# Optimization experiments

Measured on AMD Instinct MI355X. Metric: run time of the kernel, lower is better.

The kernel has to match this reference:

```python
import jax, jax.numpy as jnp
import numpy as np
import math

DIM = 256; SEQ = 2048; BSZ = 32; NI = 128; NS = 4; ITERS = 3

def _ln(x, g, b):
    m = x.mean(-1, keepdims=True)
    v = ((x - m) ** 2).mean(-1, keepdims=True)
    return (x - m) / jnp.sqrt(v + 1e-5) * g + b

def _norm(x):
    # torch F.normalize: x / ||x||.clamp_min(1e-12)
    return x / jnp.clip(jnp.linalg.norm(x, axis=-1, keepdims=True), 1e-12, None)

def setup_inputs() -> dict:
    key = jax.random.key(0)
    ks = jax.random.split(key, 16)
    def w(k, shape, s=0.02):
        return jax.random.normal(k, shape, jnp.float32) * s
    return {
        'tokens': jax.random.normal(ks[0], (BSZ, SEQ, DIM), jnp.float32),
        'cls_embed': jax.random.normal(ks[1], (BSZ, DIM), jnp.float32),
        'intent_queries': jax.random.normal(ks[2], (NI, DIM), jnp.float32),
        'noise': jax.random.normal(ks[3], (NI, BSZ, NS, DIM), jnp.float32),
        'Wk': w(ks[4], (DIM, DIM)), 'bk': jnp.zeros(DIM, jnp.float32),
        'Wv': w(ks[5], (DIM, DIM)), 'bv': jnp.zeros(DIM, jnp.float32),
        'Wqs': w(ks[6], (DIM, DIM)), 'bqs': jnp.zeros(DIM, jnp.float32),
        'Wqi': w(ks[7], (DIM, DIM)), 'bqi': jnp.zeros(DIM, jnp.float32),
        'ln1_g': jnp.ones(DIM, jnp.float32), 'ln1_b': jnp.zeros(DIM, jnp.float32),
        'ln2_g': jnp.ones(DIM, jnp.float32), 'ln2_b': jnp.zeros(DIM, jnp.float32),
        'Wf1': w(ks[8], (DIM, 2 * DIM)), 'bf1': jnp.zeros(2 * DIM, jnp.float32),
        'Wf2': w(ks[9], (2 * DIM, DIM)), 'bf2': jnp.zeros(DIM, jnp.float32),
        'slot_mu': w(ks[10], (1, NS, DIM)),  # randn*0.02
        'slot_sigma': jnp.ones((1, NS, DIM), jnp.float32) * 0.1,
        'alpha': jnp.float32(1.0),
        'temperature': jnp.float32(1.0),
    }

def reference(tokens, cls_embed, intent_queries, noise, Wk, bk, Wv, bv,
              Wqs, bqs, Wqi, bqi, ln1_g, ln1_b, ln2_g, ln2_b,
              Wf1, bf1, Wf2, bf2, slot_mu, slot_sigma, alpha, temperature):
    scale = 1.0 / math.sqrt(DIM)
    # k/v are identical across the per-intent loop in the original -> compute once
    k = tokens @ Wk + bk  # [B,S,D]
    v = tokens @ Wv + bv  # [B,S,D]
    cls_n = _norm(cls_embed)  # [B,D]

    def per_intent(q, eps):  # q: [D], eps: [B,NS,D]
        qn = _norm(q)
        q_intent = (q @ Wqi + bqi)[None, None, :]  # broadcast over [B,NS,:]
        slots = slot_mu[0] + eps * slot_sigma[0]   # [B,NS,D]
        for _ in range(ITERS):
            q_slot = slots @ Wqs + bqs + q_intent
            logit = jnp.einsum('bnd,bsd->bns', q_slot, k) * scale
            attn = jax.nn.softmax(logit, axis=-1)
            upd = jnp.einsum('bns,bsd->bnd', attn, v)
            slots = _ln(slots + upd, ln1_g, ln1_b)
            h = _ln(slots, ln2_g, ln2_b)
            slots = slots + jax.nn.gelu(h @ Wf1 + bf1, approximate=False) @ Wf2 + bf2
        sn = _norm(slots)                               # [B,NS,D]
        a = jax.nn.softmax(jnp.einsum('bnd,d->bn', sn, qn), axis=-1)
        summ = jnp.einsum('bn,bnd->bd', a, slots)       # slot_summary
        fused = cls_n + alpha * _norm(summ)
        return fused @ qn                               # [B]

    scores = jax.vmap(per_intent)(intent_queries, noise)  # [NI,B]
    logits = scores.T / jnp.maximum(temperature, 1e-4)    # [B,NI]
    return logits
```

## Files before the change

### kernel.cpp

```cpp
#include <hip/hip_runtime.h>
#include <math.h>

#define BSZ 32
#define NI  128

typedef __attribute__((ext_vector_type(8))) _Float16 f16x8;
typedef __attribute__((ext_vector_type(4))) _Float16 f16x4;
typedef __attribute__((ext_vector_type(4))) float    f32x4;

#define MFMA16(a, b, c) __builtin_amdgcn_mfma_f32_16x16x32_f16((a), (b), (c), 0, 0, 0)

#define GLL(g, l) __builtin_amdgcn_global_load_lds(                          \
    (const __attribute__((address_space(1))) void*)(g),                      \
    (__attribute__((address_space(3))) void*)(l), 16, 0, 0)

#define LGKM_BAR() do {                                                      \
    asm volatile("s_waitcnt lgkmcnt(0)" ::: "memory");                       \
    __builtin_amdgcn_sched_barrier(0);                                       \
    __builtin_amdgcn_s_barrier();                                            \
    __builtin_amdgcn_sched_barrier(0); } while (0)

__device__ inline float dot4f(float4 a, float4 b) {
    return a.x * b.x + a.y * b.y + a.z * b.z + a.w * b.w;
}

__device__ inline float4* slp(float* base, int r, int c) {
    return (float4*)(base + r * 256 + ((((c) >> 2) ^ (r & 7)) << 2));
}

__device__ inline void tpose64(const float* __restrict__ src, int Csrc,
                               _Float16* __restrict__ dstT, int KT,
                               int r0, int c0, _Float16 (*tbuf)[72], int tid)
{
#pragma unroll
    for (int it = 0; it < 4; it++) {
        int idx = tid + it * 256;
        int rr = idx >> 4, c4 = idx & 15;
        float4 w = *(const float4*)(src + (size_t)(r0 + rr) * Csrc + c0 + c4 * 4);
        tbuf[c4 * 4 + 0][rr] = (_Float16)w.x;
        tbuf[c4 * 4 + 1][rr] = (_Float16)w.y;
        tbuf[c4 * 4 + 2][rr] = (_Float16)w.z;
        tbuf[c4 * 4 + 3][rr] = (_Float16)w.w;
    }
    __syncthreads();
#pragma unroll
    for (int it = 0; it < 2; it++) {
        int idx = tid + it * 256;
        int orr = idx >> 3, oc8 = idx & 7;
        int n = c0 + orr;
        size_t tile = (size_t)(n >> 4) * KT + (r0 >> 5) + (oc8 >> 2);
        *(f16x8*)(dstT + tile * 512 + (n & 15) * 32 + (oc8 & 3) * 8) = *(const f16x8*)&tbuf[orr][oc8 * 8];
    }
}

__global__ __launch_bounds__(256) void prep(
    const float* __restrict__ Wk, const float* __restrict__ Wv,
    const float* __restrict__ Wqs, const float* __restrict__ Wf1,
    const float* __restrict__ Wf2,
    const float* __restrict__ intent_q, const float* __restrict__ Wqi,
    const float* __restrict__ bqi, const float* __restrict__ bqs,
    const float* __restrict__ cls_embed,
    _Float16* __restrict__ wkT, _Float16* __restrict__ wvT,
    _Float16* __restrict__ wqsT, _Float16* __restrict__ wf1T,
    _Float16* __restrict__ wf2T,
    float* __restrict__ qint2, float* __restrict__ qn, float* __restrict__ clsn)
{
    __shared__ _Float16 tbuf[64][72];
    __shared__ float buf[256];
    __shared__ float red[4];
    const int t = threadIdx.x, blk = blockIdx.x;
    const int lane = t & 63, w = t >> 6;

    if (blk < 112) {
        if (blk < 16)       tpose64(Wk, 256, wkT, 8, (blk >> 2) * 64, (blk & 3) * 64, tbuf, t);
        else if (blk < 32)  { int tt = blk - 16; tpose64(Wv, 256, wvT, 8, (tt >> 2) * 64, (tt & 3) * 64, tbuf, t); }
        else if (blk < 48)  { int tt = blk - 32; tpose64(Wqs, 256, wqsT, 8, (tt >> 2) * 64, (tt & 3) * 64, tbuf, t); }
        else if (blk < 80)  { int tt = blk - 48; tpose64(Wf1, 512, wf1T, 8, (tt & 3) * 64, (tt >> 2) * 64, tbuf, t); }
        else                { int tt = blk - 80; tpose64(Wf2, 256, wf2T, 16, (tt >> 2) * 64, (tt & 3) * 64, tbuf, t); }
    } else if (blk < 240) {
        int i = blk - 112;
        float x = intent_q[(size_t)i * 256 + t];
        buf[t] = x;
        float ss = x * x;
#pragma unroll
        for (int m = 1; m < 64; m <<= 1) ss += __shfl_xor(ss, m, 64);
        if (lane == 0) red[w] = ss;
        __syncthreads();
        float tot = red[0] + red[1] + red[2] + red[3];
        qn[(size_t)i * 256 + t] = x / fmaxf(sqrtf(tot), 1e-12f);
        float acc = bqi[t] + bqs[t];
        for (int e = 0; e < 256; e += 4) {
            const float4 q4 = *(const float4*)&buf[e];
            acc += q4.x * Wqi[(size_t)(e + 0) * 256 + t];
            acc += q4.y * Wqi[(size_t)(e + 1) * 256 + t];
            acc += q4.z * Wqi[(size_t)(e + 2) * 256 + t];
            acc += q4.w * Wqi[(size_t)(e + 3) * 256 + t];
        }
        qint2[(size_t)i * 256 + t] = acc;
    } else {
        int b = blk - 240;
        float x = cls_embed[(size_t)b * 256 + t];
        float ss = x * x;
#pragma unroll
        for (int m = 1; m < 64; m <<= 1) ss += __shfl_xor(ss, m, 64);
        if (lane == 0) red[w] = ss;
        __syncthreads();
        float tot = red[0] + red[1] + red[2] + red[3];
        clsn[(size_t)b * 256 + t] = x / fmaxf(sqrtf(tot), 1e-12f);
    }
}

__global__ __launch_bounds__(512, 2) void kvf_k(
    const float* __restrict__ tokens,
    const _Float16* __restrict__ wkT, const _Float16* __restrict__ wvT,
    const float* __restrict__ bk, const float* __restrict__ bv,
    _Float16* __restrict__ kT, _Float16* __restrict__ vT)
{
    __shared__ __align__(16) _Float16 Sb[2][8192];

    const int t = threadIdx.x, lane = t & 63, w = t >> 6;
    const int l15 = lane & 15, quad = lane >> 4;
    const int lofs = l15 * 32 + quad * 8;
    const int lofsA = ((l15 * 4 + quad) ^ ((l15 >> 1) & 7)) * 8;
    const int bx = blockIdx.x;
    const int b = bx & 31, chunk = bx >> 5;

    f16x8 wk[2][8], wv[2][8];
#pragma unroll
    for (int j = 0; j < 2; j++)
#pragma unroll
        for (int ks = 0; ks < 8; ks++) {
            wk[j][ks] = *(const f16x8*)(wkT + ((size_t)(2 * w + j) * 8 + ks) * 512 + lofs);
            wv[j][ks] = *(const f16x8*)(wvT + ((size_t)(2 * w + j) * 8 + ks) * 512 + lofs);
        }
    f32x4 bi0 = *(const f32x4*)(bk + w * 32 + quad * 4);
    f32x4 bi1 = *(const f32x4*)(bk + w * 32 + 16 + quad * 4);
    const float bv0 = bv[(2 * w) * 16 + l15];
    const float bv1 = bv[(2 * w + 1) * 16 + l15];

    const int rr = t >> 5, d8 = t & 31;
    const float* tbase = tokens + ((size_t)b * 2048 + chunk * 256) * 256 + rr * 256 + d8 * 8;
    const int mskW = ((rr >> 1) & 7) ^ (((d8 >> 2) & 3) << 1);
    const int wofs0 = (d8 >> 2) * 512 + (((rr * 4 + (d8 & 3)) ^ mskW) * 8);
    const int wofs1 = wofs0 + 8 * 512;

    float4 pa0, pa1, pb0, pb1;

#define KVF_LOADS(P) do {                                                    \
        const float* sp_ = tbase + (size_t)(P) * 8192;                       \
        pa0 = *(const float4*)(sp_);                                         \
        pa1 = *(const float4*)(sp_ + 4);                                     \
        pb0 = *(const float4*)(sp_ + 4096);                                  \
        pb1 = *(const float4*)(sp_ + 4100);                                  \
    } while (0)

#define KVF_STAGE(BUF) do {                                                  \
        f16x8 h0, h1;                                                        \
        h0[0] = (_Float16)pa0.x; h0[1] = (_Float16)pa0.y;                    \
        h0[2] = (_Float16)pa0.z; h0[3] = (_Float16)pa0.w;                    \
        h0[4] = (_Float16)pa1.x; h0[5] = (_Float16)pa1.y;                    \
        h0[6] = (_Float16)pa1.z; h0[7] = (_Float16)pa1.w;                    \
        h1[0] = (_Float16)pb0.x; h1[1] = (_Float16)pb0.y;                    \
        h1[2] = (_Float16)pb0.z; h1[3] = (_Float16)pb0.w;                    \
        h1[4] = (_Float16)pb1.x; h1[5] = (_Float16)pb1.y;                    \
        h1[6] = (_Float16)pb1.z; h1[7] = (_Float16)pb1.w;                    \
        *(f16x8*)((BUF) + wofs0) = h0;                                       \
        *(f16x8*)((BUF) + wofs1) = h1;                                       \
    } while (0)

    KVF_LOADS(0);
    KVF_STAGE(&Sb[0][0]);
    LGKM_BAR();

    for (int p = 0; p < 8; p++) {
        if (p < 7) KVF_LOADS(p + 1);
        __builtin_amdgcn_sched_barrier(0);

        const _Float16* lb = &Sb[p & 1][0];
        const int stg0 = chunk * 16 + p * 2;
        const int sp = chunk * 8 + p;

        f16x8 a[2][8];
#pragma unroll
        for (int st = 0; st < 2; st++)
#pragma unroll
            for (int ks = 0; ks < 8; ks++)
                a[st][ks] = *(const f16x8*)(lb + (st * 8 + ks) * 512 + (lofsA ^ ((ks & 3) * 16)));

#pragma unroll
        for (int st = 0; st < 2; st++) {
            f32x4 c0 = {0.f, 0.f, 0.f, 0.f}, c1 = {0.f, 0.f, 0.f, 0.f};
#pragma unroll
            for (int ks = 0; ks < 8; ks++) {
                c0 = MFMA16(wk[0][ks], a[st][ks], c0);
                c1 = MFMA16(wk[1][ks], a[st][ks], c1);
            }
            f16x4 p0, p1;
#pragma unroll
            for (int reg = 0; reg < 4; reg++) {
                p0[reg] = (_Float16)(c0[reg] + bi0[reg]);
                p1[reg] = (_Float16)(c1[reg] + bi1[reg]);
            }
            _Float16* tp = kT + ((size_t)(b * 128 + stg0 + st) * 8 + w) * 512 + l15 * 32;
            *(f16x4*)(tp + (quad >> 1) * 8 + (quad & 1) * 4) = p0;
            *(f16x4*)(tp + (2 + (quad >> 1)) * 8 + (quad & 1) * 4) = p1;
        }

#pragma unroll
        for (int j = 0; j < 2; j++) {
            f32x4 c0 = {0.f, 0.f, 0.f, 0.f}, c1 = {0.f, 0.f, 0.f, 0.f};
#pragma unroll
            for (int ks = 0; ks < 8; ks++) {
                c0 = MFMA16(a[0][ks], wv[j][ks], c0);
                c1 = MFMA16(a[1][ks], wv[j][ks], c1);
            }
            const float bb = j ? bv1 : bv0;
            f16x4 p0, p1;
#pragma unroll
            for (int reg = 0; reg < 4; reg++) {
                p0[reg] = (_Float16)(c0[reg] + bb);
                p1[reg] = (_Float16)(c1[reg] + bb);
            }
            _Float16* tp = vT + ((size_t)(b * 16 + 2 * w + j) * 64 + sp) * 512 + l15 * 32;
            *(f16x4*)(tp + (quad >> 1) * 8 + (quad & 1) * 4) = p0;
            *(f16x4*)(tp + (2 + (quad >> 1)) * 8 + (quad & 1) * 4) = p1;
        }

        if (p < 7) {
            KVF_STAGE(&Sb[(p + 1) & 1][0]);
            LGKM_BAR();
        }
    }
#undef KVF_LOADS
#undef KVF_STAGE
}

__global__ __launch_bounds__(256, 4) void slotq_k(
    const float* __restrict__ noise, const float* __restrict__ slot_mu,
    const float* __restrict__ slot_sigma,
    const _Float16* __restrict__ wqsT, const float* __restrict__ qint2,
    float* __restrict__ slots, _Float16* __restrict__ qsT)
{
    __shared__ float sb[16 * 256];
    const int tid = threadIdx.x, lane = tid & 63, w4 = tid >> 6;
    const int l15 = lane & 15, quad = lane >> 4;
    const int lofs = l15 * 32 + quad * 8;
    const int rt = blockIdx.x;
    const int gr0 = rt * 16;

    {
        const int lr = w4 * 4 + quad;
        const int gr = gr0 + lr;
        const int b = gr >> 9, i = (gr >> 2) & 127, n = gr & 3;
        const float* np = noise + (((size_t)i * BSZ + b) * 4 + n) * 256;
#pragma unroll
        for (int k = 0; k < 4; k++) {
            const int c = k * 64 + l15 * 4;
            float4 mu = *(const float4*)(slot_mu + n * 256 + c);
            float4 sg = *(const float4*)(slot_sigma + n * 256 + c);
            float4 ns = *(const float4*)(np + c);
            float4 o;
            o.x = mu.x + ns.x * sg.x; o.y = mu.y + ns.y * sg.y;
            o.z = mu.z + ns.z * sg.z; o.w = mu.w + ns.w * sg.w;
            *slp(sb, lr, c) = o;
            *(float4*)(slots + (size_t)gr * 256 + c) = o;
        }
    }
    __syncthreads();

    f16x8 bs[8];
#pragma unroll
    for (int ks = 0; ks < 8; ks++) {
        const int c0 = ks * 32 + quad * 8;
        float4 xa = *slp(sb, l15, c0);
        float4 xb = *slp(sb, l15, c0 + 4);
        bs[ks][0] = (_Float16)xa.x; bs[ks][1] = (_Float16)xa.y;
        bs[ks][2] = (_Float16)xa.z; bs[ks][3] = (_Float16)xa.w;
        bs[ks][4] = (_Float16)xb.x; bs[ks][5] = (_Float16)xb.y;
        bs[ks][6] = (_Float16)xb.z; bs[ks][7] = (_Float16)xb.w;
    }
    const int iq = ((gr0 + l15) & 511) >> 2;
#pragma unroll
    for (int d = 0; d < 4; d++) {
        const int dti = w4 * 4 + d;
        f32x4 c = {0.f, 0.f, 0.f, 0.f};
#pragma unroll
        for (int ks = 0; ks < 8; ks++)
            c = MFMA16(*(const f16x8*)(wqsT + ((size_t)dti * 8 + ks) * 512 + lofs), bs[ks], c);
        float4 qi = *(const float4*)(qint2 + (size_t)iq * 256 + dti * 16 + quad * 4);
        f16x4 o;
#pragma unroll
        for (int reg = 0; reg < 4; reg++) o[reg] = (_Float16)((c[reg] + qi[reg]) * 0.0625f);
        *(f16x4*)(qsT + ((size_t)rt * 8 + (dti >> 1)) * 512 + l15 * 32
                  + ((dti & 1) * 2 + (quad >> 1)) * 8 + (quad & 1) * 4) = o;
    }
}

__global__ __launch_bounds__(256, 2) void attn_k(
    const _Float16* __restrict__ qsT, const _Float16* __restrict__ kT,
    const _Float16* __restrict__ vT,
    _Float16* __restrict__ Opart, float* __restrict__ psum4)
{
    __shared__ __align__(16) _Float16 arena[24576];
    __shared__ __align__(16) _Float16 pb[4][1280];

    _Float16* KbA = arena;
    _Float16* VbA = arena + 16384;

    const int tid = threadIdx.x, lane = tid & 63, wv = tid >> 6;
    const int l15 = lane & 15, quad = lane >> 4;
    const int lofs = l15 * 32 + quad * 8;
    const int lofsA = ((l15 * 4 + quad) ^ ((l15 >> 1) & 7)) * 8;
    const int lnsw = (lane ^ ((lane >> 3) & 7)) * 8;
    const int bx = blockIdx.x;
    const int b = bx & 31, rb = (bx >> 5) & 3, sk = bx >> 7;
    const int gr0 = b * 512 + rb * 128 + wv * 32;
    const int rt_q = gr0 >> 4;

    _Float16* pw = pb[wv];

    const _Float16* kSrc = kT + ((size_t)(b * 128 + sk * 32) * 8) * 512;
    const _Float16* vSrc = vT + ((size_t)(b * 16) * 64 + sk * 16) * 512;

#pragma unroll
    for (int j = 0; j < 4; j++) {
        const int ee = wv * 4 + j;
        GLL(kSrc + (size_t)((ee >> 3) * 8 + (ee & 7)) * 512 + lnsw,
            KbA + ee * 512 + lane * 8);
    }

    f16x8 q[2][8];
#pragma unroll
    for (int m = 0; m < 2; m++)
#pragma unroll
        for (int ks = 0; ks < 8; ks++)
            q[m][ks] = *(const f16x8*)(qsT + ((size_t)(rt_q + m) * 8 + ks) * 512 + lofs);

    f32x4 O[2][16];
#pragma unroll
    for (int m = 0; m < 2; m++)
#pragma unroll
        for (int dt = 0; dt < 16; dt++) O[m][dt] = (f32x4){0.f, 0.f, 0.f, 0.f};
    float ps[2][4] = {{0.f, 0.f, 0.f, 0.f}, {0.f, 0.f, 0.f, 0.f}};

    asm volatile("s_waitcnt vmcnt(0)" ::: "memory");
    __builtin_amdgcn_s_barrier();
    __builtin_amdgcn_sched_barrier(0);

    for (int ss = 0; ss < 16; ss++) {
        const int cur = ss & 1;

#pragma unroll
        for (int j = 0; j < 4; j++) {
            const int ee = wv * 4 + j;
            GLL(vSrc + (size_t)(ee * 64 + ss) * 512 + lnsw, VbA + ee * 512 + lane * 8);
        }
        if (ss < 15) {
#pragma unroll
            for (int j = 0; j < 4; j++) {
                const int ee = wv * 4 + j;
                GLL(kSrc + (size_t)((2 * (ss + 1) + (ee >> 3)) * 8 + (ee & 7)) * 512 + lnsw,
                    KbA + (cur ^ 1) * 8192 + ee * 512 + lane * 8);
            }
            asm volatile("s_waitcnt vmcnt(8)" ::: "memory");
        } else {
            asm volatile("s_waitcnt vmcnt(4)" ::: "memory");
        }
        __builtin_amdgcn_s_barrier();
        __builtin_amdgcn_sched_barrier(0);

#pragma unroll
        for (int kt = 0; kt < 2; kt++) {
            const _Float16* kp = KbA + cur * 8192 + (kt * 8) * 512;
            f32x4 c0 = {0.f, 0.f, 0.f, 0.f}, c1 = {0.f, 0.f, 0.f, 0.f};
#pragma unroll
            for (int ks = 0; ks < 8; ks++) {
                f16x8 kf = *(const f16x8*)(kp + ks * 512 + lofsA);
                c0 = MFMA16(q[0][ks], kf, c0);
                c1 = MFMA16(q[1][ks], kf, c1);
            }
            const int col = kt * 16 + l15;
#pragma unroll
            for (int reg = 0; reg < 4; reg++) {
                float p0 = __expf(fminf(c0[reg], 10.5f));
                float p1 = __expf(fminf(c1[reg], 10.5f));
                ps[0][reg] += p0;
                ps[1][reg] += p1;
                pw[(quad * 4 + reg) * 40 + col] = (_Float16)p0;
                pw[(16 + quad * 4 + reg) * 40 + col] = (_Float16)p1;
            }
        }

        __builtin_amdgcn_sched_barrier(0);
        asm volatile("s_waitcnt lgkmcnt(0)" ::: "memory");
        if (ss < 15) {
            asm volatile("s_waitcnt vmcnt(4)" ::: "memory");
        } else {
            asm volatile("s_waitcnt vmcnt(0)" ::: "memory");
        }
        __builtin_amdgcn_s_barrier();
        __builtin_amdgcn_sched_barrier(0);

        {
            f16x8 pa0 = *(const f16x8*)(pw + l15 * 40 + quad * 8);
            f16x8 pa1 = *(const f16x8*)(pw + (16 + l15) * 40 + quad * 8);
#pragma unroll
            for (int dt = 0; dt < 16; dt++) {
                f16x8 vf = *(const f16x8*)(VbA + dt * 512 + lofsA);
                O[0][dt] = MFMA16(pa0, vf, O[0][dt]);
                O[1][dt] = MFMA16(pa1, vf, O[1][dt]);
            }
        }
        __builtin_amdgcn_sched_barrier(0);
        __builtin_amdgcn_s_barrier();
        __builtin_amdgcn_sched_barrier(0);
    }

#pragma unroll
    for (int m = 0; m < 2; m++) {
#pragma unroll
        for (int msk = 1; msk <= 8; msk <<= 1)
#pragma unroll
            for (int reg = 0; reg < 4; reg++) ps[m][reg] += __shfl_xor(ps[m][reg], msk, 64);
        if (l15 == 0) {
#pragma unroll
            for (int reg = 0; reg < 4; reg++)
                psum4[(size_t)sk * 16384 + gr0 + m * 16 + quad * 4 + reg] = ps[m][reg];
        }
    }

    _Float16* ow = arena + wv * 2176;
#pragma unroll
    for (int m = 0; m < 2; m++) {
#pragma unroll
        for (int hd = 0; hd < 2; hd++) {
#pragma unroll
            for (int dt = 0; dt < 8; dt++) {
                const int dti = hd * 8 + dt;
#pragma unroll
                for (int reg = 0; reg < 4; reg++)
                    ow[(quad * 4 + reg) * 136 + dt * 16 + l15] = (_Float16)O[m][dti][reg];
            }
#pragma unroll
            for (int p2 = 0; p2 < 4; p2++) {
                const int u = lane + p2 * 64;
                const int row = u >> 4, col8 = u & 15;
                *(f16x8*)(Opart + ((size_t)sk * 16384 + gr0 + m * 16 + row) * 256 + hd * 128 + col8 * 8) =
                    *(const f16x8*)(ow + row * 136 + col8 * 8);
            }
        }
    }
}

__global__ __launch_bounds__(256, 2) void mlp_k(
    const _Float16* __restrict__ Opart, const float* __restrict__ psum4,
    float* __restrict__ slots,
    const float* __restrict__ ln1_g, const float* __restrict__ ln1_b,
    const float* __restrict__ ln2_g, const float* __restrict__ ln2_b,
    const _Float16* __restrict__ wf1T, const float* __restrict__ bf1,
    const _Float16* __restrict__ wf2T, const float* __restrict__ bf2,
    const _Float16* __restrict__ wqsT, const float* __restrict__ qint2,
    _Float16* __restrict__ qsT,
    const float* __restrict__ qn, const float* __restrict__ clsn,
    const float* __restrict__ alphap, const float* __restrict__ tempp,
    float* __restrict__ out, int it)
{
    __shared__ float sl[32 * 256];
    __shared__ float2 st2[32];
    __shared__ __align__(16) _Float16 actL[16384];

    const int tid = threadIdx.x, lane = tid & 63, w4 = tid >> 6;
    const int l15 = lane & 15, quad = lane >> 4;
    const int lofs = l15 * 32 + quad * 8;
    const int lofsA = ((l15 * 4 + quad) ^ ((l15 >> 1) & 7)) * 8;
    const int bx = blockIdx.x;
    const int b = bx & 31, rg = bx >> 5;
    const int R0 = b * 512 + rg * 32;

#pragma unroll
    for (int r2 = 0; r2 < 2; r2++) {
        const int lr = w4 * 8 + r2 * 4 + quad;
        const int gr = R0 + lr;
        float l = 0.f;
#pragma unroll
        for (int j = 0; j < 4; j++) l += psum4[(size_t)j * 16384 + gr];
        const float invl = 1.f / l;
        float4 y[4];
        float sm = 0.f, sq = 0.f;
#pragma unroll
        for (int k = 0; k < 4; k++) {
            const int c = k * 64 + l15 * 4;
            float4 o4 = {0.f, 0.f, 0.f, 0.f};
#pragma unroll
            for (int j = 0; j < 4; j++) {
                f16x4 p = *(const f16x4*)(Opart + ((size_t)j * 16384 + gr) * 256 + c);
                o4.x += (float)p[0]; o4.y += (float)p[1];
                o4.z += (float)p[2]; o4.w += (float)p[3];
            }
            float4 s4 = *(const float4*)(slots + (size_t)gr * 256 + c);
            y[k].x = s4.x + o4.x * invl; y[k].y = s4.y + o4.y * invl;
            y[k].z = s4.z + o4.z * invl; y[k].w = s4.w + o4.w * invl;
            sm += y[k].x + y[k].y + y[k].z + y[k].w;
            sq += dot4f(y[k], y[k]);
        }
#pragma unroll
        for (int m = 1; m <= 8; m <<= 1) { sm += __shfl_xor(sm, m, 64); sq += __shfl_xor(sq, m, 64); }
        const float mean = sm * (1.f / 256.f);
        const float rstd = rsqrtf(sq * (1.f / 256.f) - mean * mean + 1e-5f);
        float sm2 = 0.f, sq2 = 0.f;
#pragma unroll
        for (int k = 0; k < 4; k++) {
            const int c = k * 64 + l15 * 4;
            float4 g1 = *(const float4*)(ln1_g + c);
            float4 b1 = *(const float4*)(ln1_b + c);
            float4 x1;
            x1.x = (y[k].x - mean) * rstd * g1.x + b1.x;
            x1.y = (y[k].y - mean) * rstd * g1.y + b1.y;
            x1.z = (y[k].z - mean) * rstd * g1.z + b1.z;
            x1.w = (y[k].w - mean) * rstd * g1.w + b1.w;
            *slp(sl, lr, c) = x1;
            sm2 += x1.x + x1.y + x1.z + x1.w;
            sq2 += dot4f(x1, x1);
        }
#pragma unroll
        for (int m = 1; m <= 8; m <<= 1) { sm2 += __shfl_xor(sm2, m, 64); sq2 += __shfl_xor(sq2, m, 64); }
        const float mean2 = sm2 * (1.f / 256.f);
        const float rstd2 = rsqrtf(sq2 * (1.f / 256.f) - mean2 * mean2 + 1e-5f);
        if (l15 == 0) st2[lr] = make_float2(mean2, rstd2);
    }
    __syncthreads();

    {
        f16x8 bh[2][8];
#pragma unroll
        for (int tt = 0; tt < 2; tt++) {
            const float2 s2 = st2[tt * 16 + l15];
#pragma unroll
            for (int ks = 0; ks < 8; ks++) {
                const int c0 = ks * 32 + quad * 8;
                float4 xa = *slp(sl, tt * 16 + l15, c0);
                float4 xb = *slp(sl, tt * 16 + l15, c0 + 4);
                float4 ga = *(const float4*)(ln2_g + c0);
                float4 gb = *(const float4*)(ln2_g + c0 + 4);
                float4 ba = *(const float4*)(ln2_b + c0);
                float4 bb2 = *(const float4*)(ln2_b + c0 + 4);
                bh[tt][ks][0] = (_Float16)((xa.x - s2.x) * s2.y * ga.x + ba.x);
                bh[tt][ks][1] = (_Float16)((xa.y - s2.x) * s2.y * ga.y + ba.y);
                bh[tt][ks][2] = (_Float16)((xa.z - s2.x) * s2.y * ga.z + ba.z);
                bh[tt][ks][3] = (_Float16)((xa.w - s2.x) * s2.y * ga.w + ba.w);
                bh[tt][ks][4] = (_Float16)((xb.x - s2.x) * s2.y * gb.x + bb2.x);
                bh[tt][ks][5] = (_Float16)((xb.y - s2.x) * s2.y * gb.y + bb2.y);
                bh[tt][ks][6] = (_Float16)((xb.z - s2.x) * s2.y * gb.z + bb2.z);
                bh[tt][ks][7] = (_Float16)((xb.w - s2.x) * s2.y * gb.w + bb2.w);
            }
        }
#pragma unroll 2
        for (int t8 = 0; t8 < 8; t8++) {
            const int hti = w4 * 8 + t8;
            f32x4 c0 = {0.f, 0.f, 0.f, 0.f}, c1 = {0.f, 0.f, 0.f, 0.f};
#pragma unroll
            for (int ks = 0; ks < 8; ks++) {
                f16x8 wfrag = *(const f16x8*)(wf1T + ((size_t)hti * 8 + ks) * 512 + lofs);
                c0 = MFMA16(wfrag, bh[0][ks], c0);
                c1 = MFMA16(wfrag, bh[1][ks], c1);
            }
            float4 bb = *(const float4*)(bf1 + hti * 16 + quad * 4);
            f16x4 o0, o1;
#pragma unroll
            for (int reg = 0; reg < 4; reg++) {
                float xg0 = c0[reg] + bb[reg];
                float xg1 = c1[reg] + bb[reg];
                o0[reg] = (_Float16)(0.5f * xg0 * (1.f + erff(xg0 * 0.70710678118654752f)));
                o1[reg] = (_Float16)(0.5f * xg1 * (1.f + erff(xg1 * 0.70710678118654752f)));
            }
            const int gA = l15 * 4 + (hti & 1) * 2 + (quad >> 1);
            const int aofs = ((size_t)(hti >> 1)) * 512 + ((gA ^ ((l15 >> 1) & 7)) * 8) + (quad & 1) * 4;
            *(f16x4*)(actL + aofs) = o0;
            *(f16x4*)(actL + 8192 + aofs) = o1;
        }
    }
    __syncthreads();

    {
        f32x4 c[2][4];
#pragma unroll
        for (int tt = 0; tt < 2; tt++)
#pragma unroll
            for (int d = 0; d < 4; d++) {
                const int dti = w4 * 4 + d;
                float4 x4 = *slp(sl, tt * 16 + l15, dti * 16 + quad * 4);
                float4 bb = *(const float4*)(bf2 + dti * 16 + quad * 4);
                c[tt][d] = (f32x4){x4.x + bb.x, x4.y + bb.y, x4.z + bb.z, x4.w + bb.w};
            }
        for (int ks = 0; ks < 16; ks++) {
            f16x8 a0 = *(const f16x8*)(actL + (size_t)ks * 512 + lofsA);
            f16x8 a1 = *(const f16x8*)(actL + 8192 + (size_t)ks * 512 + lofsA);
#pragma unroll
            for (int d = 0; d < 4; d++) {
                f16x8 wfrag = *(const f16x8*)(wf2T + ((size_t)(w4 * 4 + d) * 16 + ks) * 512 + lofs);
                c[0][d] = MFMA16(wfrag, a0, c[0][d]);
                c[1][d] = MFMA16(wfrag, a1, c[1][d]);
            }
        }
        __syncthreads();
#pragma unroll
        for (int tt = 0; tt < 2; tt++)
#pragma unroll
            for (int d = 0; d < 4; d++) {
                const int dti = w4 * 4 + d;
                float4 v = {c[tt][d][0], c[tt][d][1], c[tt][d][2], c[tt][d][3]};
                *slp(sl, tt * 16 + l15, dti * 16 + quad * 4) = v;
            }
    }
    __syncthreads();

    if (it < 2) {
        f16x8 bs[2][8];
#pragma unroll
        for (int tt = 0; tt < 2; tt++)
#pragma unroll
            for (int ks = 0; ks < 8; ks++) {
                const int c0 = ks * 32 + quad * 8;
                float4 xa = *slp(sl, tt * 16 + l15, c0);
                float4 xb = *slp(sl, tt * 16 + l15, c0 + 4);
                bs[tt][ks][0] = (_Float16)xa.x; bs[tt][ks][1] = (_Float16)xa.y;
                bs[tt][ks][2] = (_Float16)xa.z; bs[tt][ks][3] = (_Float16)xa.w;
                bs[tt][ks][4] = (_Float16)xb.x; bs[tt][ks][5] = (_Float16)xb.y;
                bs[tt][ks][6] = (_Float16)xb.z; bs[tt][ks][7] = (_Float16)xb.w;
            }
        const int iq0 = rg * 8 + (l15 >> 2);
        const int rtg0 = b * 32 + rg * 2;
#pragma unroll
        for (int d = 0; d < 4; d++) {
            const int dti = w4 * 4 + d;
            f32x4 c0 = {0.f, 0.f, 0.f, 0.f}, c1 = {0.f, 0.f, 0.f, 0.f};
#pragma unroll
            for (int ks = 0; ks < 8; ks++) {
                f16x8 wfrag = *(const f16x8*)(wqsT + ((size_t)dti * 8 + ks) * 512 + lofs);
                c0 = MFMA16(wfrag, bs[0][ks], c0);
                c1 = MFMA16(wfrag, bs[1][ks], c1);
            }
            float4 qi0 = *(const float4*)(qint2 + (size_t)iq0 * 256 + dti * 16 + quad * 4);
            float4 qi1 = *(const float4*)(qint2 + (size_t)(iq0 + 4) * 256 + dti * 16 + quad * 4);
            f16x4 o0, o1;
#pragma unroll
            for (int reg = 0; reg < 4; reg++) {
                o0[reg] = (_Float16)((c0[reg] + qi0[reg]) * 0.0625f);
                o1[reg] = (_Float16)((c1[reg] + qi1[reg]) * 0.0625f);
            }
            const int qofs = (dti >> 1) * 512 + l15 * 32
                           + ((dti & 1) * 2 + (quad >> 1)) * 8 + (quad & 1) * 4;
            *(f16x4*)(qsT + (size_t)rtg0 * 4096 + qofs) = o0;
            *(f16x4*)(qsT + (size_t)(rtg0 + 1) * 4096 + qofs) = o1;
        }
        {
            const int lr2 = tid >> 3, k8 = tid & 7;
#pragma unroll
            for (int q4 = 0; q4 < 8; q4++) {
                float4 v = *slp(sl, lr2, k8 * 32 + q4 * 4);
                *(float4*)(slots + (size_t)(R0 + lr2) * 256 + k8 * 32 + q4 * 4) = v;
            }
        }
    } else {
#pragma unroll
        for (int ii = 0; ii < 2; ii++) {
            const int i_loc = w4 * 2 + ii;
            const int i = rg * 8 + i_loc;
            float4 qv = *(const float4*)(qn + (size_t)i * 256 + lane * 4);
            float4 xs[4];
            float st4[4];
#pragma unroll
            for (int n = 0; n < 4; n++) {
                xs[n] = *slp(sl, i_loc * 4 + n, lane * 4);
                float ss = dot4f(xs[n], xs[n]);
                float sq = dot4f(xs[n], qv);
#pragma unroll
                for (int m = 1; m < 64; m <<= 1) { ss += __shfl_xor(ss, m, 64); sq += __shfl_xor(sq, m, 64); }
                st4[n] = sq / fmaxf(sqrtf(ss), 1e-12f);
            }
            float mx = fmaxf(fmaxf(st4[0], st4[1]), fmaxf(st4[2], st4[3]));
            float e0 = __expf(st4[0] - mx), e1 = __expf(st4[1] - mx);
            float e2 = __expf(st4[2] - mx), e3 = __expf(st4[3] - mx);
            float inv = 1.f / (e0 + e1 + e2 + e3);
            float4 smv;
            smv.x = (e0 * xs[0].x + e1 * xs[1].x + e2 * xs[2].x + e3 * xs[3].x) * inv;
            smv.y = (e0 * xs[0].y + e1 * xs[1].y + e2 * xs[2].y + e3 * xs[3].y) * inv;
            smv.z = (e0 * xs[0].z + e1 * xs[1].z + e2 * xs[2].z + e3 * xs[3].z) * inv;
            smv.w = (e0 * xs[0].w + e1 * xs[1].w + e2 * xs[2].w + e3 * xs[3].w) * inv;
            float ssm = dot4f(smv, smv);
            float sqn = dot4f(smv, qv);
            float4 cv = *(const float4*)(clsn + (size_t)b * 256 + lane * 4);
            float cq = dot4f(cv, qv);
#pragma unroll
            for (int m = 1; m < 64; m <<= 1) {
                ssm += __shfl_xor(ssm, m, 64);
                sqn += __shfl_xor(sqn, m, 64);
                cq  += __shfl_xor(cq,  m, 64);
            }
            if (lane == 0) {
                float score = cq + alphap[0] * sqn / fmaxf(sqrtf(ssm), 1e-12f);
                out[(size_t)b * NI + i] = score / fmaxf(tempp[0], 1e-4f);
            }
        }
    }
}

extern "C" void kernel_launch(void* const* d_in, const int* in_sizes, int n_in,
                              void* d_out, int out_size, void* d_ws, size_t ws_size,
                              hipStream_t stream)
{
    const float* tokens     = (const float*)d_in[0];
    const float* cls_embed  = (const float*)d_in[1];
    const float* intent_q   = (const float*)d_in[2];
    const float* noise      = (const float*)d_in[3];
    const float* Wk  = (const float*)d_in[4];
    const float* bk  = (const float*)d_in[5];
    const float* Wv  = (const float*)d_in[6];
    const float* bv  = (const float*)d_in[7];
    const float* Wqs = (const float*)d_in[8];
    const float* bqs = (const float*)d_in[9];
    const float* Wqi = (const float*)d_in[10];
    const float* bqi = (const float*)d_in[11];
    const float* ln1g = (const float*)d_in[12];
    const float* ln1b = (const float*)d_in[13];
    const float* ln2g = (const float*)d_in[14];
    const float* ln2b = (const float*)d_in[15];
    const float* Wf1 = (const float*)d_in[16];
    const float* bf1 = (const float*)d_in[17];
    const float* Wf2 = (const float*)d_in[18];
    const float* bf2 = (const float*)d_in[19];
    const float* slot_mu    = (const float*)d_in[20];
    const float* slot_sigma = (const float*)d_in[21];
    const float* alphap = (const float*)d_in[22];
    const float* tempp  = (const float*)d_in[23];
    float* out = (float*)d_out;

    char* base = (char*)d_ws;
    _Float16* qsT   = (_Float16*)(base);
    _Float16* kT    = (_Float16*)(base + 33554432u);
    _Float16* vT    = (_Float16*)(base + 67108864u);
    _Float16* Opart = (_Float16*)(base + 100663296u);
    float* slots    = (float*)(base + 134217728u);
    _Float16* wkT   = (_Float16*)(base + 150994944u);
    _Float16* wvT   = (_Float16*)(base + 151126016u);
    _Float16* wqsT  = (_Float16*)(base + 151257088u);
    _Float16* wf1T  = (_Float16*)(base + 151388160u);
    _Float16* wf2T  = (_Float16*)(base + 151650304u);
    float* qint2    = (float*)(base + 151912448u);
    float* qnb      = (float*)(base + 152043520u);
    float* clsn     = (float*)(base + 152174592u);
    float* psum4    = (float*)(base + 152207360u);

    prep<<<272, 256, 0, stream>>>(Wk, Wv, Wqs, Wf1, Wf2, intent_q, Wqi, bqi, bqs,
                                  cls_embed, wkT, wvT, wqsT, wf1T, wf2T,
                                  qint2, qnb, clsn);
    kvf_k<<<256, 512, 0, stream>>>(tokens, wkT, wvT, bk, bv, kT, vT);
    slotq_k<<<1024, 256, 0, stream>>>(noise, slot_mu, slot_sigma, wqsT, qint2,
                                      slots, qsT);

    for (int it = 0; it < 3; it++) {
        attn_k<<<512, 256, 0, stream>>>(qsT, kT, vT, Opart, psum4);
        mlp_k<<<512, 256, 0, stream>>>(Opart, psum4, slots,
                                       ln1g, ln1b, ln2g, ln2b,
                                       wf1T, bf1, wf2T, bf2,
                                       wqsT, qint2, qsT,
                                       qnb, clsn, alphap, tempp, out, it);
    }
}
```

Measured before the change: 438.1 us.

## Double-buffer V tiles alongside K and drop per-step barriers in attention loop

The attention kernel now double-buffers both K and V tiles in LDS, prefetching the next step's K and V together. This lets it drop two of the three per-iteration vmcnt waits and barriers, leaving a single wait-and-barrier at the end of each step. The aim is to hide V load latency behind the QK and PV MFMA work and cut synchronisation stalls. In exchange LDS use grows from 24K to 32K halves plus the P buffers, which may reduce occupancy at 2 blocks per CU.

New measurement: 435.6 us. Within noise of the previous version (-0.6%).

```diff
diff --git a/kernel.cpp b/kernel.cpp
--- a/kernel.cpp
+++ b/kernel.cpp
@@ -301,11 +301,9 @@
     const _Float16* __restrict__ vT,
     _Float16* __restrict__ Opart, float* __restrict__ psum4)
 {
-    __shared__ __align__(16) _Float16 arena[24576];
+    __shared__ __align__(16) _Float16 KbS[2][8192];
+    __shared__ __align__(16) _Float16 VbS[2][8192];
     __shared__ __align__(16) _Float16 pb[4][1280];
-
-    _Float16* KbA = arena;
-    _Float16* VbA = arena + 16384;
 
     const int tid = threadIdx.x, lane = tid & 63, wv = tid >> 6;
     const int l15 = lane & 15, quad = lane >> 4;
@@ -326,7 +324,12 @@
     for (int j = 0; j < 4; j++) {
         const int ee = wv * 4 + j;
         GLL(kSrc + (size_t)((ee >> 3) * 8 + (ee & 7)) * 512 + lnsw,
-            KbA + ee * 512 + lane * 8);
+            KbS[0] + ee * 512 + lane * 8);
+    }
+#pragma unroll
+    for (int j = 0; j < 4; j++) {
+        const int ee = wv * 4 + j;
+        GLL(vSrc + (size_t)(ee * 64 + 0) * 512 + lnsw, VbS[0] + ee * 512 + lane * 8);
     }
 
     f16x8 q[2][8];
@@ -350,28 +353,25 @@
     for (int ss = 0; ss < 16; ss++) {
         const int cur = ss & 1;
 
-#pragma unroll
-        for (int j = 0; j < 4; j++) {
-            const int ee = wv * 4 + j;
-            GLL(vSrc + (size_t)(ee * 64 + ss) * 512 + lnsw, VbA + ee * 512 + lane * 8);
-        }
         if (ss < 15) {
 #pragma unroll
             for (int j = 0; j < 4; j++) {
                 const int ee = wv * 4 + j;
                 GLL(kSrc + (size_t)((2 * (ss + 1) + (ee >> 3)) * 8 + (ee & 7)) * 512 + lnsw,
-                    KbA + (cur ^ 1) * 8192 + ee * 512 + lane * 8);
-            }
-            asm volatile("s_waitcnt vmcnt(8)" ::: "memory");
-        } else {
-            asm volatile("s_waitcnt vmcnt(4)" ::: "memory");
-        }
-        __builtin_amdgcn_s_barrier();
+                    KbS[cur ^ 1] + ee * 512 + lane * 8);
+            }
+#pragma unroll
+            for (int j = 0; j < 4; j++) {
+                const int ee = wv * 4 + j;
+                GLL(vSrc + (size_t)(ee * 64 + (ss + 1)) * 512 + lnsw,
+                    VbS[cur ^ 1] + ee * 512 + lane * 8);
+            }
+        }
         __builtin_amdgcn_sched_barrier(0);
 
 #pragma unroll
         for (int kt = 0; kt < 2; kt++) {
-            const _Float16* kp = KbA + cur * 8192 + (kt * 8) * 512;
+            const _Float16* kp = KbS[cur] + (kt * 8) * 512;
             f32x4 c0 = {0.f, 0.f, 0.f, 0.f}, c1 = {0.f, 0.f, 0.f, 0.f};
 #pragma unroll
             for (int ks = 0; ks < 8; ks++) {
@@ -393,12 +393,6 @@
 
         __builtin_amdgcn_sched_barrier(0);
         asm volatile("s_waitcnt lgkmcnt(0)" ::: "memory");
-        if (ss < 15) {
-            asm volatile("s_waitcnt vmcnt(4)" ::: "memory");
-        } else {
-            asm volatile("s_waitcnt vmcnt(0)" ::: "memory");
-        }
-        __builtin_amdgcn_s_barrier();
         __builtin_amdgcn_sched_barrier(0);
 
         {
@@ -406,12 +400,15 @@
             f16x8 pa1 = *(const f16x8*)(pw + (16 + l15) * 40 + quad * 8);
 #pragma unroll
             for (int dt = 0; dt < 16; dt++) {
-                f16x8 vf = *(const f16x8*)(VbA + dt * 512 + lofsA);
+                f16x8 vf = *(const f16x8*)(VbS[cur] + dt * 512 + lofsA);
                 O[0][dt] = MFMA16(pa0, vf, O[0][dt]);
                 O[1][dt] = MFMA16(pa1, vf, O[1][dt]);
             }
         }
         __builtin_amdgcn_sched_barrier(0);
+        if (ss < 15) {
+            asm volatile("s_waitcnt vmcnt(0)" ::: "memory");
+        }
         __builtin_amdgcn_s_barrier();
         __builtin_amdgcn_sched_barrier(0);
     }
@@ -429,7 +426,7 @@
         }
     }
 
-    _Float16* ow = arena + wv * 2176;
+    _Float16* ow = &KbS[0][0] + wv * 2176;
 #pragma unroll
     for (int m = 0; m < 2; m++) {
 #pragma unroll
```
